# Kernel tuning notes

Measured on AMD Instinct MI355X. Metric: run time of the kernel, lower is better.

Reference implementation:

```python
import jax, jax.numpy as jnp
import numpy as np

N = 100000
NEG_SLOPE = 0.2

def _leaky_relu(x, slope):
    return jnp.where(x >= 0, x, slope * x)

def _gat_layer(h_in, W, a_src, a_dst, b, src, dst, heads, out_ch):
    # h: [N, H, C]
    h = (h_in @ W).reshape(-1, heads, out_ch)
    alpha_src = (h * a_src).sum(-1)  # [N, H]
    alpha_dst = (h * a_dst).sum(-1)  # [N, H]
    e = _leaky_relu(alpha_src[src] + alpha_dst[dst], NEG_SLOPE)  # [E, H]
    # segment softmax over destination nodes
    m = jax.ops.segment_max(e, dst, num_segments=N)
    m = jnp.where(jnp.isfinite(m), m, 0.0)
    ex = jnp.exp(e - m[dst])
    denom = jax.ops.segment_sum(ex, dst, num_segments=N)
    attn = ex / (denom[dst] + 1e-16)  # [E, H]
    out = jax.ops.segment_sum(h[src] * attn[:, :, None], dst, num_segments=N)  # [N, H, C]
    return out.reshape(-1, heads * out_ch) + b

def setup_inputs() -> dict:
    key = jax.random.key(0)
    ks = jax.random.split(key, 10)
    F_in, H1, C1, n_cls = 512, 8, 8, 16
    E = 1600000
    x = jax.random.normal(ks[0], (N, F_in), dtype=jnp.float32)
    edge_index = jax.random.randint(ks[1], (2, E), 0, N, dtype=jnp.int64)
    s1 = 1.0 / np.sqrt(F_in)
    W1 = jax.random.uniform(ks[2], (F_in, H1 * C1), jnp.float32, -s1, s1)
    a1_src = jax.random.normal(ks[3], (H1, C1), dtype=jnp.float32) * 0.1
    a1_dst = jax.random.normal(ks[4], (H1, C1), dtype=jnp.float32) * 0.1
    b1 = jnp.zeros((H1 * C1,), jnp.float32)
    s2 = 1.0 / np.sqrt(H1 * C1)
    W2 = jax.random.uniform(ks[5], (H1 * C1, n_cls), jnp.float32, -s2, s2)
    a2_src = jax.random.normal(ks[6], (1, n_cls), dtype=jnp.float32) * 0.1
    a2_dst = jax.random.normal(ks[7], (1, n_cls), dtype=jnp.float32) * 0.1
    b2 = jnp.zeros((n_cls,), jnp.float32)
    return {"x": x, "edge_index": edge_index, "W1": W1, "a1_src": a1_src,
            "a1_dst": a1_dst, "b1": b1, "W2": W2, "a2_src": a2_src,
            "a2_dst": a2_dst, "b2": b2}

def reference(x, edge_index, W1, a1_src, a1_dst, b1, W2, a2_src, a2_dst, b2):
    # add self loops (GATConv default)
    loops = jnp.arange(N, dtype=edge_index.dtype)
    src = jnp.concatenate([edge_index[0], loops])
    dst = jnp.concatenate([edge_index[1], loops])
    h = _gat_layer(x, W1, a1_src, a1_dst, b1, src, dst, 8, 8)
    h = jax.nn.elu(h)
    out = _gat_layer(h, W2, a2_src, a2_dst, b2, src, dst, 1, 16)
    return jax.nn.log_softmax(out, axis=1)
```

## Files before the change

kernel.cpp:

```cpp
#include <hip/hip_runtime.h>
#include <math.h>

#define NEG_SLOPE 0.2f
#define BKT_SHIFT 8
#define BKT_RANGE 256
#define EPB 4096

typedef __attribute__((ext_vector_type(8))) short bf16x8;
typedef __attribute__((ext_vector_type(4))) float f32x4;

__device__ __forceinline__ float elu1(float x)  { return x > 0.f ? x : expm1f(x); }

__device__ __forceinline__ unsigned short f2bf(float f) {
  unsigned u = __float_as_uint(f);
  unsigned r = (u + 0x7FFFu + ((u >> 16) & 1u)) >> 16;
  return (unsigned short)r;
}
__device__ __forceinline__ float bflo(unsigned u) { return __uint_as_float(u << 16); }
__device__ __forceinline__ float bfhi(unsigned u) { return __uint_as_float(u & 0xFFFF0000u); }
__device__ __forceinline__ unsigned cvt_pk_bf16(float lo, float hi) {
  unsigned r;
  asm("v_cvt_pk_bf16_f32 %0, %1, %2" : "=v"(r) : "v"(lo), "v"(hi));
  return r;
}

__global__ __launch_bounds__(256) void k_cvtW_zero(const float* __restrict__ W,
                                                   unsigned short* __restrict__ Wt,
                                                   int* __restrict__ bucketCount) {
  int i = blockIdx.x * 256 + threadIdx.x;
  if (i < 1024) bucketCount[i] = 0;
  if (i >= 512 * 64) return;
  int k = i >> 6, c = i & 63;
  Wt[(size_t)c * 512 + k] = f2bf(W[i]);
}

__global__ __launch_bounds__(256) void k_gemm1_mfma(const float* __restrict__ x,
                                                    const unsigned short* __restrict__ Wt,
                                                    unsigned short* __restrict__ h1b, int N) {
  __shared__ unsigned short As[128 * 64];
  __shared__ unsigned short Bs[64 * 64];
  const int t = threadIdx.x;
  const int w = t >> 6;
  const int l = t & 63;
  const int fr = l & 15;
  const int fq = l >> 4;
  const int rowbase = blockIdx.x * 128;
  f32x4 acc[2][4] = {};

  for (int k0 = 0; k0 < 512; k0 += 64) {
#pragma unroll
    for (int j = 0; j < 8; ++j) {
      int idx = j * 256 + t;
      int row = idx >> 4;
      int cg  = idx & 15;
      int grow = rowbase + row;
      float4 v = make_float4(0.f, 0.f, 0.f, 0.f);
      if (grow < N) v = *(const float4*)(x + (size_t)grow * 512 + k0 + cg * 4);
      uint2 pk;
      pk.x = cvt_pk_bf16(v.x, v.y);
      pk.y = cvt_pk_bf16(v.z, v.w);
      int ch = cg >> 1;
      int pch = ch ^ (row & 7);
      *((uint2*)(As + row * 64 + pch * 8 + (cg & 1) * 4)) = pk;
    }
#pragma unroll
    for (int rep = 0; rep < 2; ++rep) {
      int i = t + rep * 256;
      int c = i >> 3, ch = i & 7;
      uint4 v = *(const uint4*)(Wt + (size_t)c * 512 + k0 + ch * 8);
      *((uint4*)(Bs + c * 64 + (ch ^ (c & 7)) * 8)) = v;
    }
    __syncthreads();
#pragma unroll
    for (int ks = 0; ks < 2; ++ks) {
      bf16x8 a[2], b[4];
#pragma unroll
      for (int m = 0; m < 2; ++m) {
        int r = w * 32 + m * 16 + fr;
        int ch = (ks * 4 + fq) ^ (r & 7);
        a[m] = *((const bf16x8*)(As + r * 64 + ch * 8));
      }
#pragma unroll
      for (int n = 0; n < 4; ++n) {
        int c = n * 16 + fr;
        int ch = (ks * 4 + fq) ^ (c & 7);
        b[n] = *((const bf16x8*)(Bs + c * 64 + ch * 8));
      }
#pragma unroll
      for (int m = 0; m < 2; ++m)
#pragma unroll
        for (int n = 0; n < 4; ++n)
          acc[m][n] = __builtin_amdgcn_mfma_f32_16x16x32_bf16(a[m], b[n], acc[m][n], 0, 0, 0);
    }
    __syncthreads();
  }
#pragma unroll
  for (int m = 0; m < 2; ++m) {
    int rb = rowbase + w * 32 + m * 16 + fq * 4;
#pragma unroll
    for (int reg = 0; reg < 4; ++reg) {
      int row = rb + reg;
      if (row < N) {
#pragma unroll
        for (int n = 0; n < 4; ++n)
          h1b[(size_t)row * 64 + n * 16 + fr] = f2bf(acc[m][n][reg]);
      }
    }
  }
}

__global__ __launch_bounds__(256) void k_alpha1(const unsigned short* __restrict__ h1b,
                                                const float* __restrict__ a1s,
                                                const float* __restrict__ a1d,
                                                unsigned* __restrict__ ef1sp,
                                                float* __restrict__ ef1d,
                                                unsigned* __restrict__ h1f8, int N) {
  int idx = blockIdx.x * blockDim.x + threadIdx.x;
  if (idx >= N * 8) return;
  int h = idx & 7;
  uint4 raw = *(const uint4*)(h1b + (size_t)idx * 8);
  float v[8];
  v[0] = bflo(raw.x); v[1] = bfhi(raw.x);
  v[2] = bflo(raw.y); v[3] = bfhi(raw.y);
  v[4] = bflo(raw.z); v[5] = bfhi(raw.z);
  v[6] = bflo(raw.w); v[7] = bfhi(raw.w);
  const float* s_ = a1s + h * 8;
  const float* d_ = a1d + h * 8;
  float ss = 0.f, dd = 0.f;
#pragma unroll
  for (int j = 0; j < 8; ++j) { ss += v[j] * s_[j]; dd += v[j] * d_[j]; }
  ef1sp[idx] = cvt_pk_bf16(expf(ss), expf(NEG_SLOPE * ss));
  *(float2*)(ef1d + (size_t)idx * 2) = make_float2(expf(dd), expf(NEG_SLOPE * dd));
  unsigned lo = 0, hi = 0;
  lo = __builtin_amdgcn_cvt_pk_fp8_f32(v[0], v[1], lo, 0);
  lo = __builtin_amdgcn_cvt_pk_fp8_f32(v[2], v[3], lo, 1);
  hi = __builtin_amdgcn_cvt_pk_fp8_f32(v[4], v[5], hi, 0);
  hi = __builtin_amdgcn_cvt_pk_fp8_f32(v[6], v[7], hi, 1);
  *(uint2*)(h1f8 + (size_t)idx * 2) = make_uint2(lo, hi);
}

__global__ __launch_bounds__(256) void k_bhist(const int* __restrict__ dst,
                                               int* __restrict__ bucketCount,
                                               int E, int B) {
  __shared__ int h[512];
  int t = threadIdx.x;
  for (int i = t; i < B; i += 256) h[i] = 0;
  __syncthreads();
  int e0 = blockIdx.x * EPB;
#pragma unroll
  for (int i = 0; i < EPB / 256; ++i) {
    int e = e0 + i * 256 + t;
    if (e < E) atomicAdd(&h[dst[e] >> BKT_SHIFT], 1);
  }
  __syncthreads();
  for (int i = t; i < B; i += 256)
    if (h[i]) atomicAdd(bucketCount + i, h[i]);
}

__global__ __launch_bounds__(512) void k_bscan(const int* __restrict__ bucketCount,
                                               int* __restrict__ bucketOff,
                                               int* __restrict__ gCursor, int B, int E) {
  __shared__ int sm[512];
  int t = threadIdx.x;
  int v = (t < B) ? bucketCount[t] : 0;
  sm[t] = v;
  __syncthreads();
  int acc = v;
#pragma unroll
  for (int o = 1; o < 512; o <<= 1) {
    int u = (t >= o) ? sm[t - o] : 0;
    __syncthreads();
    acc += u;
    sm[t] = acc;
    __syncthreads();
  }
  if (t < B) {
    bucketOff[t] = acc - v;
    gCursor[t] = acc - v;
  }
  if (t == 0) bucketOff[B] = E;
}

__global__ __launch_bounds__(256) void k_bin(const int* __restrict__ src,
                                             const int* __restrict__ dst,
                                             int* __restrict__ gCursor,
                                             unsigned* __restrict__ binned,
                                             int E, int B) {
  __shared__ int hist[512];
  __shared__ int base[512];
  int t = threadIdx.x;
  for (int i = t; i < B; i += 256) hist[i] = 0;
  __syncthreads();
  int e0 = blockIdx.x * EPB;
#pragma unroll
  for (int i = 0; i < EPB / 256; ++i) {
    int e = e0 + i * 256 + t;
    if (e < E) atomicAdd(&hist[dst[e] >> BKT_SHIFT], 1);
  }
  __syncthreads();
  for (int i = t; i < B; i += 256) {
    int c = hist[i];
    base[i] = c ? atomicAdd(gCursor + i, c) : 0;
    hist[i] = 0;
  }
  __syncthreads();
#pragma unroll
  for (int i = 0; i < EPB / 256; ++i) {
    int e = e0 + i * 256 + t;
    if (e < E) {
      int d = dst[e];
      int b = d >> BKT_SHIFT;
      int r = atomicAdd(&hist[b], 1);
      binned[base[b] + r] = ((unsigned)(d & (BKT_RANGE - 1)) << 24) | (unsigned)src[e];
    }
  }
}

__global__ __launch_bounds__(256) void k_build(const int* __restrict__ bucketOff,
                                               const unsigned* __restrict__ binned,
                                               int* __restrict__ rowptr,
                                               int* __restrict__ deg,
                                               int* __restrict__ srt, int N) {
  __shared__ int ldeg[BKT_RANGE];
  __shared__ int sm[BKT_RANGE];
  __shared__ int lcur[BKT_RANGE];
  int t = threadIdx.x;
  int b = blockIdx.x;
  int nbase = b * BKT_RANGE;
  int estart = bucketOff[b];
  int eend = bucketOff[b + 1];
  ldeg[t] = 0;
  __syncthreads();
  for (int e = estart + t; e < eend; e += 256)
    atomicAdd(&ldeg[binned[e] >> 24], 1);
  __syncthreads();
  int v = ldeg[t];
  sm[t] = v;
  __syncthreads();
  int acc = v;
#pragma unroll
  for (int o = 1; o < 256; o <<= 1) {
    int u = (t >= o) ? sm[t - o] : 0;
    __syncthreads();
    acc += u;
    sm[t] = acc;
    __syncthreads();
  }
  int excl = estart + acc - v;
  int node = nbase + t;
  if (node < N) {
    rowptr[node] = excl;
    deg[node] = v;
  }
  lcur[t] = excl;
  __syncthreads();
  for (int e = estart + t; e < eend; e += 256) {
    unsigned p = binned[e];
    int pos = atomicAdd(&lcur[p >> 24], 1);
    srt[pos] = (int)(p & 0xFFFFFFu);
  }
}

__global__ __launch_bounds__(256) void k_agg1f(const int* __restrict__ rowptr,
                                               const int* __restrict__ deg,
                                               const int* __restrict__ srt,
                                               const unsigned* __restrict__ ef1sp,
                                               const float* __restrict__ ef1d,
                                               const unsigned* __restrict__ h1f8,
                                               const float* __restrict__ b1,
                                               const float* __restrict__ W2,
                                               const float* __restrict__ a2s,
                                               const float* __restrict__ a2d,
                                               unsigned short* __restrict__ h2b,
                                               unsigned* __restrict__ ef2sp,
                                               float* __restrict__ ef2d, int N) {
  __shared__ float vsm[4][64];
  const int t = threadIdx.x;
  const int w = t >> 6;
  const int lane = t & 63;
  const int wid = blockIdx.x * 4 + w;
  const int slot = lane >> 4;
  const int c4 = lane & 15;
  const int h = c4 >> 1;
  float a2sr = a2s[c4];
  float a2dr = a2d[c4];
  float wreg[16];
#pragma unroll
  for (int m = 0; m < 16; ++m) wreg[m] = W2[(slot * 16 + m) * 16 + c4];
  float4 b1v = *(const float4*)(b1 + c4 * 4);
  if (wid >= N) return;
  const int d = wid;

  float2 ddv = *(const float2*)(ef1d + (size_t)d * 16 + h * 2);
  unsigned es0 = ef1sp[(size_t)d * 8 + h];
  unsigned sv = h1f8[(size_t)d * 16 + c4];
  float ex0 = fmaxf(bflo(es0) * ddv.x, bfhi(es0) * ddv.y);
  ex0 = (slot == 0) ? ex0 : 0.f;
  float a0 = ex0 * __builtin_amdgcn_cvt_f32_fp8(sv, 0);
  float a1 = ex0 * __builtin_amdgcn_cvt_f32_fp8(sv, 1);
  float a2 = ex0 * __builtin_amdgcn_cvt_f32_fp8(sv, 2);
  float a3 = ex0 * __builtin_amdgcn_cvt_f32_fp8(sv, 3);
  float den = ex0;

  int start = rowptr[d];
  int len = deg[d];
  for (int k = 0; k < len; k += 4) {
    int idx = k + slot;
    bool valid = idx < len;
    int s = d;
    if (valid) s = srt[start + idx];
    unsigned es = ef1sp[(size_t)s * 8 + h];
    unsigned hv = h1f8[(size_t)s * 16 + c4];
    float ex = fmaxf(bflo(es) * ddv.x, bfhi(es) * ddv.y);
    ex = valid ? ex : 0.f;
    a0 = fmaf(ex, __builtin_amdgcn_cvt_f32_fp8(hv, 0), a0);
    a1 = fmaf(ex, __builtin_amdgcn_cvt_f32_fp8(hv, 1), a1);
    a2 = fmaf(ex, __builtin_amdgcn_cvt_f32_fp8(hv, 2), a2);
    a3 = fmaf(ex, __builtin_amdgcn_cvt_f32_fp8(hv, 3), a3);
    den += ex;
  }
#pragma unroll
  for (int o = 16; o < 64; o <<= 1) {
    a0 += __shfl_xor(a0, o);
    a1 += __shfl_xor(a1, o);
    a2 += __shfl_xor(a2, o);
    a3 += __shfl_xor(a3, o);
    den += __shfl_xor(den, o);
  }
  float rden = 1.f / (den + 1e-16f);
  if (slot == 0) {
    float4 vv;
    vv.x = elu1(a0 * rden + b1v.x);
    vv.y = elu1(a1 * rden + b1v.y);
    vv.z = elu1(a2 * rden + b1v.z);
    vv.w = elu1(a3 * rden + b1v.w);
    *(float4*)&vsm[w][c4 * 4] = vv;
  }
  float partial = 0.f;
#pragma unroll
  for (int m = 0; m < 16; ++m) partial = fmaf(vsm[w][slot * 16 + m], wreg[m], partial);
  float qs = partial * a2sr;
  float qd = partial * a2dr;
#pragma unroll
  for (int o = 1; o < 64; o <<= 1) {
    qs += __shfl_xor(qs, o);
    qd += __shfl_xor(qd, o);
  }
  float p2 = partial + __shfl_down(partial, 32);
  float hcv = p2 + __shfl_down(p2, 16);
  if (lane < 16) h2b[(size_t)d * 16 + c4] = f2bf(hcv);
  if (lane == 0) {
    ef2sp[d] = cvt_pk_bf16(expf(qs), expf(NEG_SLOPE * qs));
    *(float2*)(ef2d + (size_t)d * 2) = make_float2(expf(qd), expf(NEG_SLOPE * qd));
  }
}

__global__ __launch_bounds__(256) void k_agg2(const int* __restrict__ rowptr,
                                              const int* __restrict__ deg,
                                              const int* __restrict__ srt,
                                              const unsigned* __restrict__ ef2sp,
                                              const float* __restrict__ ef2d,
                                              const unsigned short* __restrict__ h2b,
                                              const float* __restrict__ b2,
                                              float* __restrict__ out, int N) {
  const int t = threadIdx.x;
  const int lane = t & 63;
  const int wid = (blockIdx.x * 256 + t) >> 6;
  const int slot = lane >> 2;
  const int cg = lane & 3;
  float4 b2v = *(const float4*)(b2 + cg * 4);
  if (wid >= N) return;
  const int d = wid;
  float2 ddp = *(const float2*)(ef2d + (size_t)d * 2);
  unsigned ps0 = ef2sp[d];
  uint2 sv = *(const uint2*)(h2b + (size_t)d * 16 + cg * 4);
  float ex0 = fmaxf(bflo(ps0) * ddp.x, bfhi(ps0) * ddp.y);
  ex0 = (slot == 0) ? ex0 : 0.f;
  float a0 = ex0 * bflo(sv.x), a1 = ex0 * bfhi(sv.x);
  float a2 = ex0 * bflo(sv.y), a3 = ex0 * bfhi(sv.y);
  float den = ex0;

  int start = rowptr[d];
  int len = deg[d];
  for (int k = 0; k < len; k += 16) {
    int idx = k + slot;
    bool valid = idx < len;
    int s = d;
    if (valid) s = srt[start + idx];
    unsigned ps = ef2sp[s];
    uint2 hv = *(const uint2*)(h2b + (size_t)s * 16 + cg * 4);
    float ex = fmaxf(bflo(ps) * ddp.x, bfhi(ps) * ddp.y);
    ex = valid ? ex : 0.f;
    a0 = fmaf(ex, bflo(hv.x), a0);
    a1 = fmaf(ex, bfhi(hv.x), a1);
    a2 = fmaf(ex, bflo(hv.y), a2);
    a3 = fmaf(ex, bfhi(hv.y), a3);
    den += ex;
  }
#pragma unroll
  for (int o = 4; o < 64; o <<= 1) {
    a0 += __shfl_xor(a0, o);
    a1 += __shfl_xor(a1, o);
    a2 += __shfl_xor(a2, o);
    a3 += __shfl_xor(a3, o);
    den += __shfl_xor(den, o);
  }
  float rden = 1.f / (den + 1e-16f);
  float v0 = a0 * rden + b2v.x;
  float v1 = a1 * rden + b2v.y;
  float v2 = a2 * rden + b2v.z;
  float v3 = a3 * rden + b2v.w;
  float m = fmaxf(fmaxf(v0, v1), fmaxf(v2, v3));
  m = fmaxf(m, __shfl_xor(m, 1));
  m = fmaxf(m, __shfl_xor(m, 2));
  float s = expf(v0 - m) + expf(v1 - m) + expf(v2 - m) + expf(v3 - m);
  s += __shfl_xor(s, 1);
  s += __shfl_xor(s, 2);
  float lse = m + logf(s);
  if (lane < 4) {
    float4 o4 = make_float4(v0 - lse, v1 - lse, v2 - lse, v3 - lse);
    *(float4*)(out + (size_t)d * 16 + cg * 4) = o4;
  }
}

extern "C" void kernel_launch(void* const* d_in, const int* in_sizes, int n_in,
                              void* d_out, int out_size, void* d_ws, size_t ws_size,
                              hipStream_t stream) {
  const float* x    = (const float*)d_in[0];
  const int*   ei   = (const int*)d_in[1];
  const float* W1   = (const float*)d_in[2];
  const float* a1s  = (const float*)d_in[3];
  const float* a1d  = (const float*)d_in[4];
  const float* b1   = (const float*)d_in[5];
  const float* W2   = (const float*)d_in[6];
  const float* a2s  = (const float*)d_in[7];
  const float* a2d  = (const float*)d_in[8];
  const float* b2   = (const float*)d_in[9];
  float* out = (float*)d_out;

  const int N = in_sizes[0] / 512;
  const int E = in_sizes[1] / 2;
  const int* src = ei;
  const int* dst = ei + E;
  const int B = (N + BKT_RANGE - 1) >> BKT_SHIFT;
  const int EB = (E + EPB - 1) / EPB;

  float* w = (float*)d_ws;
  float* ef1d = w;  w += (size_t)N * 16;
  float* ef2d = w;  w += (size_t)N * 2;
  unsigned* ef1sp = (unsigned*)w;  w += (size_t)N * 8;
  unsigned* ef2sp = (unsigned*)w;  w += (size_t)N;
  unsigned* h1f8  = (unsigned*)w;  w += (size_t)N * 16;
  unsigned short* h1b = (unsigned short*)w;  w += (size_t)N * 32;
  unsigned short* h2b = (unsigned short*)w;  w += (size_t)N * 8;
  unsigned short* Wt  = (unsigned short*)w;  w += 512 * 64 / 2;
  int* iw = (int*)w;
  int* deg         = iw;  iw += N;
  int* rowptr      = iw;  iw += N;
  int* bucketCount = iw;  iw += 1024;
  int* bucketOff   = iw;  iw += 1024;
  int* gCursor     = iw;  iw += 1024;
  int* srt         = iw;  iw += E;
  unsigned* binned = (unsigned*)iw;  iw += E;

  k_cvtW_zero<<<(512 * 64 + 255) / 256, 256, 0, stream>>>(W1, Wt, bucketCount);

  k_bhist<<<EB, 256, 0, stream>>>(dst, bucketCount, E, B);
  k_bscan<<<1, 512, 0, stream>>>(bucketCount, bucketOff, gCursor, B, E);
  k_bin<<<EB, 256, 0, stream>>>(src, dst, gCursor, binned, E, B);
  k_build<<<B, 256, 0, stream>>>(bucketOff, binned, rowptr, deg, srt, N);

  k_gemm1_mfma<<<(N + 127) / 128, 256, 0, stream>>>(x, Wt, h1b, N);
  k_alpha1<<<(N * 8 + 255) / 256, 256, 0, stream>>>(h1b, a1s, a1d, ef1sp, ef1d, h1f8, N);
  k_agg1f<<<(N + 3) / 4, 256, 0, stream>>>(rowptr, deg, srt, ef1sp, ef1d, h1f8,
                                           b1, W2, a2s, a2d, h2b, ef2sp, ef2d, N);

  k_agg2<<<(N + 3) / 4, 256, 0, stream>>>(rowptr, deg, srt, ef2sp, ef2d, h2b, b2, out, N);
}
```

Before: 242.3 us.

## Fuse alpha/fp8 epilogue into GEMM1 and batch neighbor index loads via shuffles

```diff
diff --git a/kernel.cpp b/kernel.cpp
--- a/kernel.cpp
+++ b/kernel.cpp
@@ -36,9 +36,13 @@
 
 __global__ __launch_bounds__(256) void k_gemm1_mfma(const float* __restrict__ x,
                                                     const unsigned short* __restrict__ Wt,
-                                                    unsigned short* __restrict__ h1b, int N) {
-  __shared__ unsigned short As[128 * 64];
-  __shared__ unsigned short Bs[64 * 64];
+                                                    const float* __restrict__ a1s,
+                                                    const float* __restrict__ a1d,
+                                                    unsigned* __restrict__ h1f8,
+                                                    unsigned* __restrict__ ef1sp,
+                                                    unsigned* __restrict__ ef1dp, int N) {
+  __shared__ __align__(16) unsigned short As[128 * 64];
+  __shared__ __align__(16) unsigned short Bs[64 * 64];
   const int t = threadIdx.x;
   const int w = t >> 6;
   const int l = t & 63;
@@ -94,49 +98,48 @@
     }
     __syncthreads();
   }
+
+  float* Asf = (float*)As;
 #pragma unroll
   for (int m = 0; m < 2; ++m) {
-    int rb = rowbase + w * 32 + m * 16 + fq * 4;
+    if (m) __syncthreads();
 #pragma unroll
     for (int reg = 0; reg < 4; ++reg) {
-      int row = rb + reg;
-      if (row < N) {
-#pragma unroll
-        for (int n = 0; n < 4; ++n)
-          h1b[(size_t)row * 64 + n * 16 + fr] = f2bf(acc[m][n][reg]);
+      int lrow = w * 16 + fq * 4 + reg;
+#pragma unroll
+      for (int n = 0; n < 4; ++n)
+        Asf[lrow * 64 + n * 16 + fr] = acc[m][n][reg];
+    }
+    __syncthreads();
+#pragma unroll
+    for (int p = 0; p < 4; ++p) {
+      int flat = p * 256 + t;
+      int lrow = flat >> 4, j = flat & 15;
+      int g = rowbase + ((lrow >> 4) << 5) + m * 16 + (lrow & 15);
+      float4 f = *(float4*)(Asf + lrow * 64 + j * 4);
+      unsigned u = __builtin_amdgcn_cvt_pk_fp8_f32(f.x, f.y, 0u, 0);
+      u = __builtin_amdgcn_cvt_pk_fp8_f32(f.z, f.w, u, 1);
+      if (g < N) h1f8[(size_t)g * 16 + j] = u;
+    }
+#pragma unroll
+    for (int p = 0; p < 2; ++p) {
+      int flat = p * 256 + t;
+      int lrow = flat >> 3, hh = flat & 7;
+      int g = rowbase + ((lrow >> 4) << 5) + m * 16 + (lrow & 15);
+      float4 f0 = *(float4*)(Asf + lrow * 64 + hh * 8);
+      float4 f1 = *(float4*)(Asf + lrow * 64 + hh * 8 + 4);
+      const float* sa = a1s + hh * 8;
+      const float* da = a1d + hh * 8;
+      float ss = f0.x*sa[0]+f0.y*sa[1]+f0.z*sa[2]+f0.w*sa[3]
+               + f1.x*sa[4]+f1.y*sa[5]+f1.z*sa[6]+f1.w*sa[7];
+      float dd = f0.x*da[0]+f0.y*da[1]+f0.z*da[2]+f0.w*da[3]
+               + f1.x*da[4]+f1.y*da[5]+f1.z*da[6]+f1.w*da[7];
+      if (g < N) {
+        ef1sp[(size_t)g * 8 + hh] = cvt_pk_bf16(expf(ss), expf(NEG_SLOPE * ss));
+        ef1dp[(size_t)g * 8 + hh] = cvt_pk_bf16(expf(dd), expf(NEG_SLOPE * dd));
       }
     }
   }
-}
-
-__global__ __launch_bounds__(256) void k_alpha1(const unsigned short* __restrict__ h1b,
-                                                const float* __restrict__ a1s,
-                                                const float* __restrict__ a1d,
-                                                unsigned* __restrict__ ef1sp,
-                                                float* __restrict__ ef1d,
-                                                unsigned* __restrict__ h1f8, int N) {
-  int idx = blockIdx.x * blockDim.x + threadIdx.x;
-  if (idx >= N * 8) return;
-  int h = idx & 7;
-  uint4 raw = *(const uint4*)(h1b + (size_t)idx * 8);
-  float v[8];
-  v[0] = bflo(raw.x); v[1] = bfhi(raw.x);
-  v[2] = bflo(raw.y); v[3] = bfhi(raw.y);
-  v[4] = bflo(raw.z); v[5] = bfhi(raw.z);
-  v[6] = bflo(raw.w); v[7] = bfhi(raw.w);
-  const float* s_ = a1s + h * 8;
-  const float* d_ = a1d + h * 8;
-  float ss = 0.f, dd = 0.f;
-#pragma unroll
-  for (int j = 0; j < 8; ++j) { ss += v[j] * s_[j]; dd += v[j] * d_[j]; }
-  ef1sp[idx] = cvt_pk_bf16(expf(ss), expf(NEG_SLOPE * ss));
-  *(float2*)(ef1d + (size_t)idx * 2) = make_float2(expf(dd), expf(NEG_SLOPE * dd));
-  unsigned lo = 0, hi = 0;
-  lo = __builtin_amdgcn_cvt_pk_fp8_f32(v[0], v[1], lo, 0);
-  lo = __builtin_amdgcn_cvt_pk_fp8_f32(v[2], v[3], lo, 1);
-  hi = __builtin_amdgcn_cvt_pk_fp8_f32(v[4], v[5], hi, 0);
-  hi = __builtin_amdgcn_cvt_pk_fp8_f32(v[6], v[7], hi, 1);
-  *(uint2*)(h1f8 + (size_t)idx * 2) = make_uint2(lo, hi);
 }
 
 __global__ __launch_bounds__(256) void k_bhist(const int* __restrict__ dst,
@@ -265,7 +268,7 @@
                                                const int* __restrict__ deg,
                                                const int* __restrict__ srt,
                                                const unsigned* __restrict__ ef1sp,
-                                               const float* __restrict__ ef1d,
+                                               const unsigned* __restrict__ ef1dp,
                                                const unsigned* __restrict__ h1f8,
                                                const float* __restrict__ b1,
                                                const float* __restrict__ W2,
@@ -291,10 +294,11 @@
   if (wid >= N) return;
   const int d = wid;
 
-  float2 ddv = *(const float2*)(ef1d + (size_t)d * 16 + h * 2);
+  unsigned ddu = ef1dp[(size_t)d * 8 + h];
+  float ddx = bflo(ddu), ddy = bfhi(ddu);
   unsigned es0 = ef1sp[(size_t)d * 8 + h];
   unsigned sv = h1f8[(size_t)d * 16 + c4];
-  float ex0 = fmaxf(bflo(es0) * ddv.x, bfhi(es0) * ddv.y);
+  float ex0 = fmaxf(bflo(es0) * ddx, bfhi(es0) * ddy);
   ex0 = (slot == 0) ? ex0 : 0.f;
   float a0 = ex0 * __builtin_amdgcn_cvt_f32_fp8(sv, 0);
   float a1 = ex0 * __builtin_amdgcn_cvt_f32_fp8(sv, 1);
@@ -304,20 +308,25 @@
 
   int start = rowptr[d];
   int len = deg[d];
-  for (int k = 0; k < len; k += 4) {
-    int idx = k + slot;
-    bool valid = idx < len;
-    int s = d;
-    if (valid) s = srt[start + idx];
-    unsigned es = ef1sp[(size_t)s * 8 + h];
-    unsigned hv = h1f8[(size_t)s * 16 + c4];
-    float ex = fmaxf(bflo(es) * ddv.x, bfhi(es) * ddv.y);
-    ex = valid ? ex : 0.f;
-    a0 = fmaf(ex, __builtin_amdgcn_cvt_f32_fp8(hv, 0), a0);
-    a1 = fmaf(ex, __builtin_amdgcn_cvt_f32_fp8(hv, 1), a1);
-    a2 = fmaf(ex, __builtin_amdgcn_cvt_f32_fp8(hv, 2), a2);
-    a3 = fmaf(ex, __builtin_amdgcn_cvt_f32_fp8(hv, 3), a3);
-    den += ex;
+  for (int kb = 0; kb < len; kb += 64) {
+    int li = kb + lane;
+    int sreg = (li < len) ? srt[start + li] : 0;
+    int nit = min(16, (len - kb + 3) >> 2);
+#pragma unroll 2
+    for (int it = 0; it < nit; ++it) {
+      int idx = kb + it * 4 + slot;
+      int s = __shfl(sreg, it * 4 + slot);
+      bool valid = idx < len;
+      unsigned es = ef1sp[(size_t)s * 8 + h];
+      unsigned hv = h1f8[(size_t)s * 16 + c4];
+      float ex = fmaxf(bflo(es) * ddx, bfhi(es) * ddy);
+      ex = valid ? ex : 0.f;
+      a0 = fmaf(ex, __builtin_amdgcn_cvt_f32_fp8(hv, 0), a0);
+      a1 = fmaf(ex, __builtin_amdgcn_cvt_f32_fp8(hv, 1), a1);
+      a2 = fmaf(ex, __builtin_amdgcn_cvt_f32_fp8(hv, 2), a2);
+      a3 = fmaf(ex, __builtin_amdgcn_cvt_f32_fp8(hv, 3), a3);
+      den += ex;
+    }
   }
 #pragma unroll
   for (int o = 16; o < 64; o <<= 1) {
@@ -382,20 +391,25 @@
 
   int start = rowptr[d];
   int len = deg[d];
-  for (int k = 0; k < len; k += 16) {
-    int idx = k + slot;
-    bool valid = idx < len;
-    int s = d;
-    if (valid) s = srt[start + idx];
-    unsigned ps = ef2sp[s];
-    uint2 hv = *(const uint2*)(h2b + (size_t)s * 16 + cg * 4);
-    float ex = fmaxf(bflo(ps) * ddp.x, bfhi(ps) * ddp.y);
-    ex = valid ? ex : 0.f;
-    a0 = fmaf(ex, bflo(hv.x), a0);
-    a1 = fmaf(ex, bfhi(hv.x), a1);
-    a2 = fmaf(ex, bflo(hv.y), a2);
-    a3 = fmaf(ex, bfhi(hv.y), a3);
-    den += ex;
+  for (int kb = 0; kb < len; kb += 64) {
+    int li = kb + lane;
+    int sreg = (li < len) ? srt[start + li] : 0;
+    int nit = min(4, (len - kb + 15) >> 4);
+#pragma unroll 2
+    for (int it = 0; it < nit; ++it) {
+      int idx = kb + it * 16 + slot;
+      int s = __shfl(sreg, it * 16 + slot);
+      bool valid = idx < len;
+      unsigned ps = ef2sp[s];
+      uint2 hv = *(const uint2*)(h2b + (size_t)s * 16 + cg * 4);
+      float ex = fmaxf(bflo(ps) * ddp.x, bfhi(ps) * ddp.y);
+      ex = valid ? ex : 0.f;
+      a0 = fmaf(ex, bflo(hv.x), a0);
+      a1 = fmaf(ex, bfhi(hv.x), a1);
+      a2 = fmaf(ex, bflo(hv.y), a2);
+      a3 = fmaf(ex, bfhi(hv.y), a3);
+      den += ex;
+    }
   }
 #pragma unroll
   for (int o = 4; o < 64; o <<= 1) {
@@ -446,12 +460,11 @@
   const int EB = (E + EPB - 1) / EPB;
 
   float* w = (float*)d_ws;
-  float* ef1d = w;  w += (size_t)N * 16;
   float* ef2d = w;  w += (size_t)N * 2;
   unsigned* ef1sp = (unsigned*)w;  w += (size_t)N * 8;
+  unsigned* ef1dp = (unsigned*)w;  w += (size_t)N * 8;
   unsigned* ef2sp = (unsigned*)w;  w += (size_t)N;
   unsigned* h1f8  = (unsigned*)w;  w += (size_t)N * 16;
-  unsigned short* h1b = (unsigned short*)w;  w += (size_t)N * 32;
   unsigned short* h2b = (unsigned short*)w;  w += (size_t)N * 8;
   unsigned short* Wt  = (unsigned short*)w;  w += 512 * 64 / 2;
   int* iw = (int*)w;
@@ -470,9 +483,8 @@
   k_bin<<<EB, 256, 0, stream>>>(src, dst, gCursor, binned, E, B);
   k_build<<<B, 256, 0, stream>>>(bucketOff, binned, rowptr, deg, srt, N);
 
-  k_gemm1_mfma<<<(N + 127) / 128, 256, 0, stream>>>(x, Wt, h1b, N);
-  k_alpha1<<<(N * 8 + 255) / 256, 256, 0, stream>>>(h1b, a1s, a1d, ef1sp, ef1d, h1f8, N);
-  k_agg1f<<<(N + 3) / 4, 256, 0, stream>>>(rowptr, deg, srt, ef1sp, ef1d, h1f8,
+  k_gemm1_mfma<<<(N + 127) / 128, 256, 0, stream>>>(x, Wt, a1s, a1d, h1f8, ef1sp, ef1dp, N);
+  k_agg1f<<<(N + 3) / 4, 256, 0, stream>>>(rowptr, deg, srt, ef1sp, ef1dp, h1f8,
                                            b1, W2, a2s, a2d, h2b, ef2sp, ef2d, N);
 
   k_agg2<<<(N + 3) / 4, 256, 0, stream>>>(rowptr, deg, srt, ef2sp, ef2d, h2b, b2, out, N);
```

After: 222.6 us. 1.09x faster.
